# Optimization experiments

Hardware: AMD Instinct MI355X
Metric: run time of the kernel (lower is better)

The kernel has to match this reference:

```python
import jax, jax.numpy as jnp
import numpy as np

NUM_HEADS = 8
QKV_DIM = 32
DIM = 256
MULTI_Q = QKV_DIM * NUM_HEADS  # 256
BN_EPS = 1e-5


def conv1x1_bn(x, W, gamma, beta, mean, var):
    # 1x1 conv (no bias) followed by BatchNorm2d in eval mode.
    y = jnp.einsum('bchw,oc->bohw', x, W)
    inv = gamma / jnp.sqrt(var + BN_EPS)
    return y * inv[None, :, None, None] + (beta - mean * inv)[None, :, None, None]


def setup_inputs() -> dict:
    key = jax.random.key(0)
    ks = jax.random.split(key, 16)
    B, C, H, W = 16, DIM, 64, 64
    inp = {
        'input_': jax.random.normal(ks[0], (B, C, H, W), jnp.float32),
        'key_v_input_reduction': jax.random.normal(ks[1], (B, C, 32, 32), jnp.float32),
        # to_q: Conv2d_BN(dim -> multi_q_dim)
        'Wq': jax.random.normal(ks[2], (MULTI_Q, DIM), jnp.float32) * 0.05,
        'gq': jnp.ones((MULTI_Q,), jnp.float32),
        'bq': jnp.zeros((MULTI_Q,), jnp.float32),
        'mq': jax.random.normal(ks[3], (MULTI_Q,), jnp.float32) * 0.1,
        'vq': jax.random.uniform(ks[4], (MULTI_Q,), jnp.float32, 0.5, 1.5),
        # to_kv: Conv2d_BN(dim -> qkv_dim) (one_kv_head=True, share_kv=True)
        'Wkv': jax.random.normal(ks[5], (QKV_DIM, DIM), jnp.float32) * 0.05,
        'gkv': jnp.ones((QKV_DIM,), jnp.float32),
        'bkv': jnp.zeros((QKV_DIM,), jnp.float32),
        'mkv': jax.random.normal(ks[6], (QKV_DIM,), jnp.float32) * 0.1,
        'vkv': jax.random.uniform(ks[7], (QKV_DIM,), jnp.float32, 0.5, 1.5),
        # proj: activation -> Conv2d_BN(multi_q_dim -> dim)
        'Wp': jax.random.normal(ks[8], (DIM, MULTI_Q), jnp.float32) * 0.05,
        'gp': jnp.ones((DIM,), jnp.float32),
        'bp': jnp.zeros((DIM,), jnp.float32),
        'mp': jax.random.normal(ks[9], (DIM,), jnp.float32) * 0.1,
        'vp': jax.random.uniform(ks[10], (DIM,), jnp.float32, 0.5, 1.5),
    }
    return inp


def reference(input_, key_v_input_reduction, Wq, gq, bq, mq, vq,
              Wkv, gkv, bkv, mkv, vkv, Wp, gp, bp, mp, vp):
    B, C, H, W = input_.shape
    HW = H * W
    # Q projection -> (B, nh, d, HW)
    queries = conv1x1_bn(input_, Wq, gq, bq, mq, vq).reshape(B, NUM_HEADS, QKV_DIM, HW)
    # shared K=V projection, single kv head -> (B, 1, d, HW)
    kv = conv1x1_bn(input_, Wkv, gkv, bkv, mkv, vkv).reshape(B, 1, QKV_DIM, HW)
    key = jax.nn.softmax(kv, axis=3)       # softmax over spatial positions
    query = jax.nn.softmax(queries, axis=2)  # softmax over channel dim
    value = kv
    # context = key @ value^T : (B,1,d,d)
    context = jnp.einsum('bhdn,bhen->bhde', key, value)
    # permute(0,1,3,2) then broadcast over heads, attended = context^T @ query
    ctx_t = jnp.swapaxes(context, -1, -2)   # (B,1,d,d)
    attended = jnp.einsum('bhde,bken->bkdn'.replace('h', 'o'), ctx_t[:, 0][:, None], query) if False else jnp.matmul(ctx_t, query)  # (B,nh,d,HW) via broadcast
    attended = attended.reshape(B, MULTI_Q, H, W)
    # proj: ReLU then Conv2d_BN
    out = conv1x1_bn(jax.nn.relu(attended), Wp, gp, bp, mp, vp)
    return out
```

## Files before the change

### kernel.cpp

```cpp
#include <hip/hip_runtime.h>
#include <hip/hip_bf16.h>
#include <cstdint>

typedef _Float16 f16;
typedef _Float16 f16x4 __attribute__((ext_vector_type(4)));
typedef _Float16 f16x8 __attribute__((ext_vector_type(8)));
typedef float f32x4 __attribute__((ext_vector_type(4)));

#define MFMA16(a, b, c) __builtin_amdgcn_mfma_f32_16x16x32_f16((a), (b), (c), 0, 0, 0)

constexpr int BATCH = 16;
constexpr int C     = 256;
constexpr int HW    = 4096;
constexpr int DH    = 32;
constexpr float EPS = 1e-5f;

constexpr size_t OFF_XT = 0;
constexpr size_t SZ_XT  = (size_t)BATCH * HW * C * 2;
constexpr size_t OFF_KV = OFF_XT + SZ_XT;
constexpr size_t SZ_KV  = (size_t)BATCH * DH * HW * 4;
constexpr size_t OFF_W1 = OFF_KV + SZ_KV;
constexpr size_t OFF_B1 = OFF_W1 + 147456;
constexpr size_t OFF_WP = OFF_B1 + 2048;
constexpr size_t SZ_WP  = (size_t)C * C * 2;
constexpr size_t OFF_BP = OFF_WP + SZ_WP;
constexpr size_t OFF_RM = OFF_BP + 1024;
constexpr size_t OFF_RS = OFF_RM + 2048;
constexpr size_t OFF_U  = OFF_RS + 2048;

__device__ __forceinline__ f16x8 ld8(const f16* p) {
  f16x4 lo = *(const f16x4*)p;
  f16x4 hi = *(const f16x4*)(p + 4);
  return __builtin_shufflevector(lo, hi, 0, 1, 2, 3, 4, 5, 6, 7);
}
__device__ __forceinline__ void st8(f16* p, f16x8 v) {
  *(f16x4*)p = __builtin_shufflevector(v, v, 0, 1, 2, 3);
  *(f16x4*)(p + 4) = __builtin_shufflevector(v, v, 4, 5, 6, 7);
}

__global__ __launch_bounds__(256) void k0_prep(
    const float* __restrict__ Wq,  const float* __restrict__ gq,  const float* __restrict__ bq,
    const float* __restrict__ mq,  const float* __restrict__ vq,
    const float* __restrict__ Wkv, const float* __restrict__ gkv, const float* __restrict__ bkv,
    const float* __restrict__ mkv, const float* __restrict__ vkv,
    const float* __restrict__ Wp,  const float* __restrict__ gp,  const float* __restrict__ bp,
    const float* __restrict__ mp,  const float* __restrict__ vp,
    f16* __restrict__ WqF, float* __restrict__ b1, f16* __restrict__ WpF,
    float* __restrict__ bp2, f16* __restrict__ WkvF) {
  int id = blockIdx.x * 256 + threadIdx.x;
  if (id < 65536) {
    int j = id & 7, lane = (id >> 3) & 63, ot = (id >> 9) & 15, kc = id >> 13;
    int o = ot * 16 + (lane & 15), c = kc * 32 + ((lane >> 4) << 3) + j;
    float inv = gq[o] * rsqrtf(vq[o] + EPS);
    WqF[id] = (f16)(Wq[o * 256 + c] * inv);
  } else if (id < 131072) {
    int id2 = id - 65536;
    int j = id2 & 7, lane = (id2 >> 3) & 63, ot = (id2 >> 9) & 15, kc = id2 >> 13;
    int o = ot * 16 + (lane & 15), c = kc * 32 + ((lane >> 4) << 3) + j;
    float inv = gp[o] * rsqrtf(vp[o] + EPS);
    WpF[id2] = (f16)(Wp[o * 256 + c] * inv);
  } else if (id < 139264) {
    int id2 = id - 131072;
    int j = id2 & 7, lane = (id2 >> 3) & 63, ot = (id2 >> 9) & 1, kc = id2 >> 10;
    int o = ot * 16 + (lane & 15), c = kc * 32 + ((lane >> 4) << 3) + j;
    float inv = gkv[o] * rsqrtf(vkv[o] + EPS);
    WkvF[id2] = (f16)(Wkv[o * 256 + c] * inv);
  } else if (id < 139552) {
    int r = id - 139264;
    if (r < 256) { float inv = gq[r] * rsqrtf(vq[r] + EPS);   b1[r] = bq[r] - mq[r] * inv; }
    else { int e = r - 256; float inv = gkv[e] * rsqrtf(vkv[e] + EPS); b1[r] = bkv[e] - mkv[e] * inv; }
  } else if (id < 139808) {
    int o = id - 139552;
    float inv = gp[o] * rsqrtf(vp[o] + EPS);
    bp2[o] = bp[o] - mp[o] * inv;
  }
}

__global__ __launch_bounds__(256, 4) void p0_trans_kv(
    const float* __restrict__ X, const f16* __restrict__ WkvF, const float* __restrict__ bkv1,
    f16* __restrict__ XTF, float* __restrict__ kvo) {
  __shared__ alignas(16) f16 xt[64 * 260];
  float* kvb = (float*)xt;
  const int t = threadIdx.x, b = blockIdx.y, n0 = blockIdx.x * 64;
  const int lane = t & 63, w = t >> 6, l15 = lane & 15, quad = lane >> 4;
  const float* Xb = X + (size_t)b * C * HW;

  {
    int c4 = (t & 15) * 4, n4 = (t >> 4) * 4;
#pragma unroll
    for (int ci = 0; ci < 4; ++ci) {
      int c0 = ci * 64 + c4;
      const float* xp = Xb + (size_t)c0 * HW + n0 + n4;
      float4 v0 = *(const float4*)&xp[0];
      float4 v1 = *(const float4*)&xp[HW];
      float4 v2 = *(const float4*)&xp[2 * HW];
      float4 v3 = *(const float4*)&xp[3 * HW];
      f16x4 w0 = {(f16)v0.x, (f16)v1.x, (f16)v2.x, (f16)v3.x};
      f16x4 w1 = {(f16)v0.y, (f16)v1.y, (f16)v2.y, (f16)v3.y};
      f16x4 w2 = {(f16)v0.z, (f16)v1.z, (f16)v2.z, (f16)v3.z};
      f16x4 w3 = {(f16)v0.w, (f16)v1.w, (f16)v2.w, (f16)v3.w};
      *(f16x4*)&xt[(n4 + 0) * 260 + c0] = w0;
      *(f16x4*)&xt[(n4 + 1) * 260 + c0] = w1;
      *(f16x4*)&xt[(n4 + 2) * 260 + c0] = w2;
      *(f16x4*)&xt[(n4 + 3) * 260 + c0] = w3;
    }
  }
  __syncthreads();

  {
    f16* XFt = XTF + ((size_t)b * 64 + blockIdx.x) * 16384;
#pragma unroll
    for (int i = 0; i < 8; ++i) {
      int u = t + i * 256;
      int l15u = u & 15, qdu = (u >> 4) & 3, ntu = (u >> 6) & 3, kcu = u >> 8;
      f16x8 v = ld8(&xt[(ntu * 16 + l15u) * 260 + kcu * 32 + qdu * 8]);
      *(f16x8*)&XFt[(size_t)u * 8] = v;
    }
  }

  f32x4 acc0, acc1;
  {
    float bv0 = bkv1[l15], bv1 = bkv1[16 + l15];
#pragma unroll
    for (int r = 0; r < 4; ++r) { acc0[r] = bv0; acc1[r] = bv1; }
  }
#pragma unroll
  for (int kc = 0; kc < 8; ++kc) {
    f16x8 af  = ld8(&xt[(w * 16 + l15) * 260 + kc * 32 + quad * 8]);
    f16x8 bf0 = *(const f16x8*)&WkvF[((size_t)(kc * 2 + 0) * 64 + lane) * 8];
    f16x8 bf1 = *(const f16x8*)&WkvF[((size_t)(kc * 2 + 1) * 64 + lane) * 8];
    acc0 = MFMA16(af, bf0, acc0);
    acc1 = MFMA16(af, bf1, acc1);
  }
  __syncthreads();
#pragma unroll
  for (int r = 0; r < 4; ++r) {
    int n = w * 16 + quad * 4 + r;
    kvb[l15 * 68 + n] = acc0[r];
    kvb[(16 + l15) * 68 + n] = acc1[r];
  }
  __syncthreads();
#pragma unroll
  for (int i = 0; i < 2; ++i) {
    int u = t + i * 256, d = u >> 4, seg = u & 15;
    float4 v = *(const float4*)&kvb[d * 68 + seg * 4];
    *(float4*)&kvo[((size_t)b * DH + d) * HW + n0 + seg * 4] = v;
  }
}

__global__ __launch_bounds__(256) void k2_stats(
    const float* __restrict__ kv, float* __restrict__ rowmax, float* __restrict__ rowsum) {
  int r = blockIdx.x, t = threadIdx.x, w = t >> 6, lane = t & 63;
  const float4* row = (const float4*)(kv + (size_t)r * HW);
  float4 v0 = row[t], v1 = row[t + 256], v2 = row[t + 512], v3 = row[t + 768];
  float m = fmaxf(fmaxf(fmaxf(v0.x, v0.y), fmaxf(v0.z, v0.w)),
                  fmaxf(fmaxf(v1.x, v1.y), fmaxf(v1.z, v1.w)));
  m = fmaxf(m, fmaxf(fmaxf(fmaxf(v2.x, v2.y), fmaxf(v2.z, v2.w)),
                     fmaxf(fmaxf(v3.x, v3.y), fmaxf(v3.z, v3.w))));
  for (int off = 32; off; off >>= 1) m = fmaxf(m, __shfl_xor(m, off));
  __shared__ float sm[4], ss[4];
  if (lane == 0) sm[w] = m;
  __syncthreads();
  m = fmaxf(fmaxf(sm[0], sm[1]), fmaxf(sm[2], sm[3]));
  float s = __expf(v0.x - m) + __expf(v0.y - m) + __expf(v0.z - m) + __expf(v0.w - m)
          + __expf(v1.x - m) + __expf(v1.y - m) + __expf(v1.z - m) + __expf(v1.w - m)
          + __expf(v2.x - m) + __expf(v2.y - m) + __expf(v2.z - m) + __expf(v2.w - m)
          + __expf(v3.x - m) + __expf(v3.y - m) + __expf(v3.z - m) + __expf(v3.w - m);
  for (int off = 32; off; off >>= 1) s += __shfl_xor(s, off);
  if (lane == 0) ss[w] = s;
  __syncthreads();
  if (t == 0) { rowmax[r] = m; rowsum[r] = ss[0] + ss[1] + ss[2] + ss[3]; }
}

__global__ __launch_bounds__(256, 4) void k3_ctx(
    const float* __restrict__ kv, const float* __restrict__ rowmax,
    const float* __restrict__ rowsum, float* __restrict__ U) {
  __shared__ float cacc[32 * 33];
  const int t = threadIdx.x, b = blockIdx.y;
  const int lane = t & 63, w = t >> 6, l15 = lane & 15, quad = lane >> 4;
  for (int i = t; i < 32 * 33; i += 256) cacc[i] = 0.f;
  __syncthreads();
  const float* kvb = kv + (size_t)b * DH * HW;
  float M0 = rowmax[b * 32 + l15],      Si0 = 1.f / rowsum[b * 32 + l15];
  float M1 = rowmax[b * 32 + 16 + l15], Si1 = 1.f / rowsum[b * 32 + 16 + l15];
  f32x4 acc[2][2] = {};
#pragma unroll
  for (int s = 0; s < 2; ++s) {
    int nb = blockIdx.x * 256 + w * 64 + s * 32 + quad * 8;
    const float* p0 = &kvb[(size_t)l15 * HW + nb];
    const float* p1 = &kvb[(size_t)(16 + l15) * HW + nb];
    float lo[8], hi[8];
    *(float4*)&lo[0] = *(const float4*)&p0[0]; *(float4*)&lo[4] = *(const float4*)&p0[4];
    *(float4*)&hi[0] = *(const float4*)&p1[0]; *(float4*)&hi[4] = *(const float4*)&p1[4];
    f16x8 A0, A1, B0, B1;
#pragma unroll
    for (int j = 0; j < 8; ++j) {
      A0[j] = (f16)lo[j]; A1[j] = (f16)hi[j];
      B0[j] = (f16)(__expf(lo[j] - M0) * Si0);
      B1[j] = (f16)(__expf(hi[j] - M1) * Si1);
    }
    acc[0][0] = MFMA16(A0, B0, acc[0][0]);
    acc[1][0] = MFMA16(A1, B0, acc[1][0]);
    acc[0][1] = MFMA16(A0, B1, acc[0][1]);
    acc[1][1] = MFMA16(A1, B1, acc[1][1]);
  }
#pragma unroll
  for (int a = 0; a < 2; ++a)
#pragma unroll
    for (int e2 = 0; e2 < 2; ++e2)
#pragma unroll
      for (int r = 0; r < 4; ++r)
        atomicAdd(&cacc[(a * 16 + quad * 4 + r) * 33 + e2 * 16 + l15], acc[a][e2][r]);
  __syncthreads();
  for (int i = t; i < 1024; i += 256)
    atomicAdd(&U[b * 1024 + (i >> 5) * 32 + (i & 31)], cacc[(i >> 5) * 33 + (i & 31)]);
}

__global__ __launch_bounds__(256, 3) void kb_mega(
    const f16* __restrict__ XTF, const f16* __restrict__ WqF, const float* __restrict__ bq1,
    const float* __restrict__ U, const f16* __restrict__ WpF, const float* __restrict__ bp1,
    float* __restrict__ out) {
  __shared__ alignas(16) f16 pa[64 * 260];
  __shared__ alignas(16) f16 ctxs[32 * 36];
  const int t = threadIdx.x, b = blockIdx.y, n0 = blockIdx.x * 64;
  const int lane = t & 63, w = t >> 6, l15 = lane & 15, quad = lane >> 4;
  const int wn = w & 1, wm = w >> 1;

  {
    const float4 u4 = *(const float4*)&U[b * 1024 + t * 4];
    int d = t >> 3, e4 = (t & 7) * 4;
    f16x4 pk = {(f16)u4.x, (f16)u4.y, (f16)u4.z, (f16)u4.w};
    *(f16x4*)&ctxs[d * 36 + e4] = pk;
  }

  f32x4 acc1[2][8];
#pragma unroll
  for (int nf = 0; nf < 8; ++nf) {
    float bv = bq1[wn * 128 + nf * 16 + l15];
#pragma unroll
    for (int mf = 0; mf < 2; ++mf)
#pragma unroll
      for (int r = 0; r < 4; ++r) acc1[mf][nf][r] = bv;
  }
  {
    const f16* XF = XTF + ((size_t)b * 64 + blockIdx.x) * 16384;
    const f16* xb = XF + ((size_t)(wm * 2) * 64 + lane) * 8;
    const f16* wb = WqF + ((size_t)(wn * 8) * 64 + lane) * 8;
    f16x8 va0 = *(const f16x8*)&xb[0];
    f16x8 va1 = *(const f16x8*)&xb[512];
    f16x8 vw[8];
#pragma unroll
    for (int nf = 0; nf < 8; ++nf) vw[nf] = *(const f16x8*)&wb[nf * 512];
#pragma unroll 1
    for (int kc = 0; kc < 8; ++kc) {
      f16x8 na0, na1, nw[8];
      if (kc < 7) {
        const f16* xb2 = xb + (kc + 1) * 2048;
        const f16* wb2 = wb + (kc + 1) * 8192;
        na0 = *(const f16x8*)&xb2[0];
        na1 = *(const f16x8*)&xb2[512];
#pragma unroll
        for (int nf = 0; nf < 8; ++nf) nw[nf] = *(const f16x8*)&wb2[nf * 512];
      }
#pragma unroll
      for (int nf = 0; nf < 8; ++nf) {
        acc1[0][nf] = MFMA16(va0, vw[nf], acc1[0][nf]);
        acc1[1][nf] = MFMA16(va1, vw[nf], acc1[1][nf]);
      }
      va0 = na0; va1 = na1;
#pragma unroll
      for (int nf = 0; nf < 8; ++nf) vw[nf] = nw[nf];
    }
  }

#pragma unroll
  for (int mf = 0; mf < 2; ++mf)
#pragma unroll
    for (int h = 0; h < 4; ++h) {
      f32x4 v0 = acc1[mf][h * 2], v1 = acc1[mf][h * 2 + 1];
      f32x4 mx;
#pragma unroll
      for (int r = 0; r < 4; ++r) mx[r] = fmaxf(v0[r], v1[r]);
#pragma unroll
      for (int off = 1; off <= 8; off <<= 1)
#pragma unroll
        for (int r = 0; r < 4; ++r) mx[r] = fmaxf(mx[r], __shfl_xor(mx[r], off));
      f32x4 s4;
#pragma unroll
      for (int r = 0; r < 4; ++r) {
        v0[r] = __expf(v0[r] - mx[r]); v1[r] = __expf(v1[r] - mx[r]);
        s4[r] = v0[r] + v1[r];
      }
#pragma unroll
      for (int off = 1; off <= 8; off <<= 1)
#pragma unroll
        for (int r = 0; r < 4; ++r) s4[r] += __shfl_xor(s4[r], off);
      int o0 = wn * 128 + h * 32 + l15;
#pragma unroll
      for (int r = 0; r < 4; ++r) {
        int n = wm * 32 + mf * 16 + quad * 4 + r;
        float si = 1.f / s4[r];
        pa[n * 260 + o0]      = (f16)(v0[r] * si);
        pa[n * 260 + o0 + 16] = (f16)(v1[r] * si);
      }
    }
  __syncthreads();

  f32x4 datt[2][2][4] = {};
#pragma unroll
  for (int hh = 0; hh < 2; ++hh) {
    int h = w * 2 + hh;
#pragma unroll
    for (int mt = 0; mt < 2; ++mt) {
      f16x8 af = ld8(&ctxs[(mt * 16 + l15) * 36 + quad * 8]);
#pragma unroll
      for (int nt = 0; nt < 4; ++nt) {
        f16x8 bf = ld8(&pa[(nt * 16 + l15) * 260 + h * 32 + quad * 8]);
        datt[hh][mt][nt] = MFMA16(af, bf, datt[hh][mt][nt]);
      }
    }
  }
#pragma unroll
  for (int hh = 0; hh < 2; ++hh) {
    int h = w * 2 + hh;
#pragma unroll
    for (int mt = 0; mt < 2; ++mt)
#pragma unroll
      for (int nt = 0; nt < 4; ++nt)
#pragma unroll
        for (int r = 0; r < 4; ++r) {
          int n = nt * 16 + l15;
          int cc = h * 32 + mt * 16 + quad * 4 + r;
          pa[n * 260 + cc] = (f16)fmaxf(datt[hh][mt][nt][r], 0.f);
        }
  }
  __syncthreads();

  f32x4 acc2[8][2];
#pragma unroll
  for (int mf = 0; mf < 8; ++mf)
#pragma unroll
    for (int r = 0; r < 4; ++r) {
      float bv = bp1[wm * 128 + mf * 16 + quad * 4 + r];
      acc2[mf][0][r] = bv; acc2[mf][1][r] = bv;
    }
  {
    const f16* wb = WpF + ((size_t)(wm * 8) * 64 + lane) * 8;
    f16x8 vw[8];
#pragma unroll
    for (int mf = 0; mf < 8; ++mf) vw[mf] = *(const f16x8*)&wb[mf * 512];
#pragma unroll 1
    for (int kc = 0; kc < 8; ++kc) {
      f16x8 nw[8];
      if (kc < 7) {
        const f16* wb2 = wb + (kc + 1) * 8192;
#pragma unroll
        for (int mf = 0; mf < 8; ++mf) nw[mf] = *(const f16x8*)&wb2[mf * 512];
      }
      f16x8 bf0 = ld8(&pa[(wn * 32 + l15) * 260 + kc * 32 + quad * 8]);
      f16x8 bf1 = ld8(&pa[(wn * 32 + 16 + l15) * 260 + kc * 32 + quad * 8]);
#pragma unroll
      for (int mf = 0; mf < 8; ++mf) {
        acc2[mf][0] = MFMA16(vw[mf], bf0, acc2[mf][0]);
        acc2[mf][1] = MFMA16(vw[mf], bf1, acc2[mf][1]);
      }
#pragma unroll
      for (int mf = 0; mf < 8; ++mf) vw[mf] = nw[mf];
    }
  }
#pragma unroll
  for (int mf = 0; mf < 8; ++mf)
#pragma unroll
    for (int nf = 0; nf < 2; ++nf) {
      int n = n0 + wn * 32 + nf * 16 + l15;
#pragma unroll
      for (int r = 0; r < 4; ++r) {
        int o = wm * 128 + mf * 16 + quad * 4 + r;
        out[((size_t)b * C + o) * HW + n] = acc2[mf][nf][r];
      }
    }
}

extern "C" void kernel_launch(void* const* d_in, const int* in_sizes, int n_in,
                              void* d_out, int out_size, void* d_ws, size_t ws_size,
                              hipStream_t stream) {
  (void)in_sizes; (void)n_in; (void)out_size; (void)ws_size;
  const float* input = (const float*)d_in[0];
  const float* Wq  = (const float*)d_in[2];
  const float* gq  = (const float*)d_in[3];
  const float* bq  = (const float*)d_in[4];
  const float* mq  = (const float*)d_in[5];
  const float* vq  = (const float*)d_in[6];
  const float* Wkv = (const float*)d_in[7];
  const float* gkv = (const float*)d_in[8];
  const float* bkv = (const float*)d_in[9];
  const float* mkv = (const float*)d_in[10];
  const float* vkv = (const float*)d_in[11];
  const float* Wp  = (const float*)d_in[12];
  const float* gp  = (const float*)d_in[13];
  const float* bp  = (const float*)d_in[14];
  const float* mp  = (const float*)d_in[15];
  const float* vp  = (const float*)d_in[16];

  char* ws = (char*)d_ws;
  f16*   XTF = (f16*)(ws + OFF_XT);
  float* kvw = (float*)(ws + OFF_KV);
  f16*   WqF = (f16*)(ws + OFF_W1);
  f16*   WkvF= (f16*)(ws + OFF_W1 + 131072);
  float* b1  = (float*)(ws + OFF_B1);
  f16*   WpF = (f16*)(ws + OFF_WP);
  float* bp2 = (float*)(ws + OFF_BP);
  float* rm  = (float*)(ws + OFF_RM);
  float* rs  = (float*)(ws + OFF_RS);
  float* U   = (float*)(ws + OFF_U);
  float* out = (float*)d_out;

  const float* bq1  = b1;
  const float* bkv1 = b1 + 256;

  hipMemsetAsync(U, 0, (size_t)BATCH * DH * DH * 4, stream);
  k0_prep<<<547, 256, 0, stream>>>(Wq, gq, bq, mq, vq, Wkv, gkv, bkv, mkv, vkv,
                                   Wp, gp, bp, mp, vp, WqF, b1, WpF, bp2, WkvF);
  p0_trans_kv<<<dim3(64, 16), 256, 0, stream>>>(input, WkvF, bkv1, XTF, kvw);
  k2_stats<<<512, 256, 0, stream>>>(kvw, rm, rs);
  k3_ctx<<<dim3(16, 16), 256, 0, stream>>>(kvw, rm, rs, U);
  kb_mega<<<dim3(64, 16), 256, 0, stream>>>(XTF, WqF, bq1, U, WpF, bp2, out);
}
```

Before: 208.3 us.

## Fuse softmax row stats into KV projection and drop memset kernel

Computes per-tile partial max and sum-of-exp for the spatial softmax inside the KV projection kernel, and combines the 64 partials per row at the start of the context kernel. This removes the separate stats kernel and its full re-read of the KV buffer. The memset of U moves into the prep kernel, and s_setprio hints are placed around the MFMA loops in the mega kernel. The transpose thread mapping is also swapped. The partial-softmax combine adds a little work per context block and some extra workspace.

New measurement: 203.6 us. 1.02x faster.

```diff
diff --git a/kernel.cpp b/kernel.cpp
--- a/kernel.cpp
+++ b/kernel.cpp
@@ -24,18 +24,14 @@
 constexpr size_t OFF_WP = OFF_B1 + 2048;
 constexpr size_t SZ_WP  = (size_t)C * C * 2;
 constexpr size_t OFF_BP = OFF_WP + SZ_WP;
-constexpr size_t OFF_RM = OFF_BP + 1024;
-constexpr size_t OFF_RS = OFF_RM + 2048;
-constexpr size_t OFF_U  = OFF_RS + 2048;
+constexpr size_t OFF_U  = OFF_BP + 1024;
+constexpr size_t OFF_PM = OFF_U + 65536;
+constexpr size_t OFF_PS = OFF_PM + 131072;
 
 __device__ __forceinline__ f16x8 ld8(const f16* p) {
   f16x4 lo = *(const f16x4*)p;
   f16x4 hi = *(const f16x4*)(p + 4);
   return __builtin_shufflevector(lo, hi, 0, 1, 2, 3, 4, 5, 6, 7);
-}
-__device__ __forceinline__ void st8(f16* p, f16x8 v) {
-  *(f16x4*)p = __builtin_shufflevector(v, v, 0, 1, 2, 3);
-  *(f16x4*)(p + 4) = __builtin_shufflevector(v, v, 4, 5, 6, 7);
 }
 
 __global__ __launch_bounds__(256) void k0_prep(
@@ -46,7 +42,7 @@
     const float* __restrict__ Wp,  const float* __restrict__ gp,  const float* __restrict__ bp,
     const float* __restrict__ mp,  const float* __restrict__ vp,
     f16* __restrict__ WqF, float* __restrict__ b1, f16* __restrict__ WpF,
-    float* __restrict__ bp2, f16* __restrict__ WkvF) {
+    float* __restrict__ bp2, f16* __restrict__ WkvF, float* __restrict__ U) {
   int id = blockIdx.x * 256 + threadIdx.x;
   if (id < 65536) {
     int j = id & 7, lane = (id >> 3) & 63, ot = (id >> 9) & 15, kc = id >> 13;
@@ -73,12 +69,15 @@
     int o = id - 139552;
     float inv = gp[o] * rsqrtf(vp[o] + EPS);
     bp2[o] = bp[o] - mp[o] * inv;
+  } else if (id < 139808 + 16384) {
+    U[id - 139808] = 0.f;
   }
 }
 
 __global__ __launch_bounds__(256, 4) void p0_trans_kv(
     const float* __restrict__ X, const f16* __restrict__ WkvF, const float* __restrict__ bkv1,
-    f16* __restrict__ XTF, float* __restrict__ kvo) {
+    f16* __restrict__ XTF, float* __restrict__ kvo,
+    float* __restrict__ pmax, float* __restrict__ psum) {
   __shared__ alignas(16) f16 xt[64 * 260];
   float* kvb = (float*)xt;
   const int t = threadIdx.x, b = blockIdx.y, n0 = blockIdx.x * 64;
@@ -86,7 +85,7 @@
   const float* Xb = X + (size_t)b * C * HW;
 
   {
-    int c4 = (t & 15) * 4, n4 = (t >> 4) * 4;
+    int n4 = (t & 15) * 4, c4 = (t >> 4) * 4;
 #pragma unroll
     for (int ci = 0; ci < 4; ++ci) {
       int c0 = ci * 64 + c4;
@@ -146,43 +145,62 @@
     float4 v = *(const float4*)&kvb[d * 68 + seg * 4];
     *(float4*)&kvo[((size_t)b * DH + d) * HW + n0 + seg * 4] = v;
   }
-}
-
-__global__ __launch_bounds__(256) void k2_stats(
-    const float* __restrict__ kv, float* __restrict__ rowmax, float* __restrict__ rowsum) {
-  int r = blockIdx.x, t = threadIdx.x, w = t >> 6, lane = t & 63;
-  const float4* row = (const float4*)(kv + (size_t)r * HW);
-  float4 v0 = row[t], v1 = row[t + 256], v2 = row[t + 512], v3 = row[t + 768];
-  float m = fmaxf(fmaxf(fmaxf(v0.x, v0.y), fmaxf(v0.z, v0.w)),
-                  fmaxf(fmaxf(v1.x, v1.y), fmaxf(v1.z, v1.w)));
-  m = fmaxf(m, fmaxf(fmaxf(fmaxf(v2.x, v2.y), fmaxf(v2.z, v2.w)),
-                     fmaxf(fmaxf(v3.x, v3.y), fmaxf(v3.z, v3.w))));
-  for (int off = 32; off; off >>= 1) m = fmaxf(m, __shfl_xor(m, off));
-  __shared__ float sm[4], ss[4];
-  if (lane == 0) sm[w] = m;
-  __syncthreads();
-  m = fmaxf(fmaxf(sm[0], sm[1]), fmaxf(sm[2], sm[3]));
-  float s = __expf(v0.x - m) + __expf(v0.y - m) + __expf(v0.z - m) + __expf(v0.w - m)
-          + __expf(v1.x - m) + __expf(v1.y - m) + __expf(v1.z - m) + __expf(v1.w - m)
-          + __expf(v2.x - m) + __expf(v2.y - m) + __expf(v2.z - m) + __expf(v2.w - m)
-          + __expf(v3.x - m) + __expf(v3.y - m) + __expf(v3.z - m) + __expf(v3.w - m);
-  for (int off = 32; off; off >>= 1) s += __shfl_xor(s, off);
-  if (lane == 0) ss[w] = s;
-  __syncthreads();
-  if (t == 0) { rowmax[r] = m; rowsum[r] = ss[0] + ss[1] + ss[2] + ss[3]; }
+
+  {
+    int d = t >> 3, j = t & 7;
+    float vals[8];
+#pragma unroll
+    for (int q = 0; q < 8; ++q) vals[q] = kvb[d * 68 + j * 8 + q];
+    float m = vals[0];
+#pragma unroll
+    for (int q = 1; q < 8; ++q) m = fmaxf(m, vals[q]);
+#pragma unroll
+    for (int off = 1; off <= 4; off <<= 1) m = fmaxf(m, __shfl_xor(m, off));
+    float s = 0.f;
+#pragma unroll
+    for (int q = 0; q < 8; ++q) s += __expf(vals[q] - m);
+#pragma unroll
+    for (int off = 1; off <= 4; off <<= 1) s += __shfl_xor(s, off);
+    if (j == 0) {
+      pmax[((size_t)b * DH + d) * 64 + blockIdx.x] = m;
+      psum[((size_t)b * DH + d) * 64 + blockIdx.x] = s;
+    }
+  }
 }
 
 __global__ __launch_bounds__(256, 4) void k3_ctx(
-    const float* __restrict__ kv, const float* __restrict__ rowmax,
-    const float* __restrict__ rowsum, float* __restrict__ U) {
+    const float* __restrict__ kv, const float* __restrict__ pmax,
+    const float* __restrict__ psum, float* __restrict__ U) {
   __shared__ float cacc[32 * 33];
+  __shared__ float Ms[32], SiS[32];
   const int t = threadIdx.x, b = blockIdx.y;
   const int lane = t & 63, w = t >> 6, l15 = lane & 15, quad = lane >> 4;
   for (int i = t; i < 32 * 33; i += 256) cacc[i] = 0.f;
-  __syncthreads();
+
+  {
+    int i = t >> 3, j = t & 7;
+    const float* pm = pmax + ((size_t)b * DH + i) * 64 + j * 8;
+    const float* ps = psum + ((size_t)b * DH + i) * 64 + j * 8;
+    float mv[8], sv[8];
+#pragma unroll
+    for (int q = 0; q < 8; ++q) { mv[q] = pm[q]; sv[q] = ps[q]; }
+    float M = mv[0];
+#pragma unroll
+    for (int q = 1; q < 8; ++q) M = fmaxf(M, mv[q]);
+#pragma unroll
+    for (int off = 1; off <= 4; off <<= 1) M = fmaxf(M, __shfl_xor(M, off));
+    float S = 0.f;
+#pragma unroll
+    for (int q = 0; q < 8; ++q) S += sv[q] * __expf(mv[q] - M);
+#pragma unroll
+    for (int off = 1; off <= 4; off <<= 1) S += __shfl_xor(S, off);
+    if (j == 0) { Ms[i] = M; SiS[i] = 1.f / S; }
+  }
+  __syncthreads();
+
   const float* kvb = kv + (size_t)b * DH * HW;
-  float M0 = rowmax[b * 32 + l15],      Si0 = 1.f / rowsum[b * 32 + l15];
-  float M1 = rowmax[b * 32 + 16 + l15], Si1 = 1.f / rowsum[b * 32 + 16 + l15];
+  float M0 = Ms[l15],      Si0 = SiS[l15];
+  float M1 = Ms[16 + l15], Si1 = SiS[16 + l15];
   f32x4 acc[2][2] = {};
 #pragma unroll
   for (int s = 0; s < 2; ++s) {
@@ -262,11 +280,13 @@
 #pragma unroll
         for (int nf = 0; nf < 8; ++nf) nw[nf] = *(const f16x8*)&wb2[nf * 512];
       }
+      __builtin_amdgcn_s_setprio(1);
 #pragma unroll
       for (int nf = 0; nf < 8; ++nf) {
         acc1[0][nf] = MFMA16(va0, vw[nf], acc1[0][nf]);
         acc1[1][nf] = MFMA16(va1, vw[nf], acc1[1][nf]);
       }
+      __builtin_amdgcn_s_setprio(0);
       va0 = na0; va1 = na1;
 #pragma unroll
       for (int nf = 0; nf < 8; ++nf) vw[nf] = nw[nf];
@@ -313,11 +333,13 @@
 #pragma unroll
     for (int mt = 0; mt < 2; ++mt) {
       f16x8 af = ld8(&ctxs[(mt * 16 + l15) * 36 + quad * 8]);
+      __builtin_amdgcn_s_setprio(1);
 #pragma unroll
       for (int nt = 0; nt < 4; ++nt) {
         f16x8 bf = ld8(&pa[(nt * 16 + l15) * 260 + h * 32 + quad * 8]);
         datt[hh][mt][nt] = MFMA16(af, bf, datt[hh][mt][nt]);
       }
+      __builtin_amdgcn_s_setprio(0);
     }
   }
 #pragma unroll
@@ -359,11 +381,13 @@
       }
       f16x8 bf0 = ld8(&pa[(wn * 32 + l15) * 260 + kc * 32 + quad * 8]);
       f16x8 bf1 = ld8(&pa[(wn * 32 + 16 + l15) * 260 + kc * 32 + quad * 8]);
+      __builtin_amdgcn_s_setprio(1);
 #pragma unroll
       for (int mf = 0; mf < 8; ++mf) {
         acc2[mf][0] = MFMA16(vw[mf], bf0, acc2[mf][0]);
         acc2[mf][1] = MFMA16(vw[mf], bf1, acc2[mf][1]);
       }
+      __builtin_amdgcn_s_setprio(0);
 #pragma unroll
       for (int mf = 0; mf < 8; ++mf) vw[mf] = nw[mf];
     }
@@ -410,19 +434,17 @@
   float* b1  = (float*)(ws + OFF_B1);
   f16*   WpF = (f16*)(ws + OFF_WP);
   float* bp2 = (float*)(ws + OFF_BP);
-  float* rm  = (float*)(ws + OFF_RM);
-  float* rs  = (float*)(ws + OFF_RS);
   float* U   = (float*)(ws + OFF_U);
+  float* pm  = (float*)(ws + OFF_PM);
+  float* ps  = (float*)(ws + OFF_PS);
   float* out = (float*)d_out;
 
   const float* bq1  = b1;
   const float* bkv1 = b1 + 256;
 
-  hipMemsetAsync(U, 0, (size_t)BATCH * DH * DH * 4, stream);
-  k0_prep<<<547, 256, 0, stream>>>(Wq, gq, bq, mq, vq, Wkv, gkv, bkv, mkv, vkv,
-                                   Wp, gp, bp, mp, vp, WqF, b1, WpF, bp2, WkvF);
-  p0_trans_kv<<<dim3(64, 16), 256, 0, stream>>>(input, WkvF, bkv1, XTF, kvw);
-  k2_stats<<<512, 256, 0, stream>>>(kvw, rm, rs);
-  k3_ctx<<<dim3(16, 16), 256, 0, stream>>>(kvw, rm, rs, U);
+  k0_prep<<<611, 256, 0, stream>>>(Wq, gq, bq, mq, vq, Wkv, gkv, bkv, mkv, vkv,
+                                   Wp, gp, bp, mp, vp, WqF, b1, WpF, bp2, WkvF, U);
+  p0_trans_kv<<<dim3(64, 16), 256, 0, stream>>>(input, WkvF, bkv1, XTF, kvw, pm, ps);
+  k3_ctx<<<dim3(16, 16), 256, 0, stream>>>(kvw, pm, ps, U);
   kb_mega<<<dim3(64, 16), 256, 0, stream>>>(XTF, WqF, bq1, U, WpF, bp2, out);
 }
```
